# Performance work log

Hardware: AMD Instinct MI355X
Metric: run time of the kernel (lower is better)

Reference implementation:

```python
import jax, jax.numpy as jnp
import numpy as np


def setup_inputs() -> dict:
    key = jax.random.key(0)
    k1, k2 = jax.random.split(key)
    G, T, H, E, C = 8, 4096, 1024, 32, 64
    token_inputs = jax.random.normal(k1, (G, T, H), dtype=jnp.float32)
    W = jax.random.normal(k2, (H, E), dtype=jnp.float32) * 0.02  # default_kernel_init stddev
    b = jnp.zeros((E,), dtype=jnp.float32)
    return {"token_inputs": token_inputs, "W": W, "b": b,
            "num_experts": E, "expert_capacity": C}


def reference(token_inputs, W, b, num_experts, expert_capacity):
    # RouterWeights: dense projection to expert logits, computed in fp32.
    x = token_inputs.astype(jnp.float32)                      # [G, T, H]
    router_logits = jnp.einsum('gth,he->gte', x, W) + b        # [G, T, E]
    router_probs = jax.nn.softmax(router_logits, axis=-1)      # [G, T, E]

    # Experts-choose masked routing: each expert picks its top-C tokens.
    probs_et = jnp.swapaxes(router_probs, 1, 2)                # [G, E, T]
    gate, idx = jax.lax.top_k(probs_et, expert_capacity)       # [G, E, C]

    T = token_inputs.shape[1]
    # one-hot over the token axis -> dispatch mask [G, T, E, C]
    dispatch = jax.nn.one_hot(idx, T, dtype=jnp.float32)       # [G, E, C, T]
    dispatch = jnp.transpose(dispatch, (0, 3, 1, 2))           # [G, T, E, C]
    combine = dispatch * gate[:, None, :, :]                   # [G, T, E, C]

    # Router z-loss on raw logits.
    G_, T_, _ = router_logits.shape
    log_z = jax.nn.logsumexp(router_logits, axis=-1)           # [G, T]
    z_loss = jnp.sum(jnp.square(log_z), dtype=jnp.float32) / (G_ * T_)
    return combine, dispatch, z_loss
```

## Files before the change

kernel.cpp:

```cpp
#include <hip/hip_runtime.h>
#include <math.h>

#define G 8
#define T 4096
#define H 1024
#define E 32
#define C 64
#define NTOK (G*T)
#define COMBINE_SZ ((size_t)G*T*E*C)
#define KC 64
#define TBLK 128

__global__ __launch_bounds__(256) void k_router(
    const float* __restrict__ x, const float* __restrict__ W,
    const float* __restrict__ bias, float* __restrict__ probs_t,
    float* __restrict__ z_out)
{
    __shared__ float xs[TBLK][68];
    __shared__ float ws2[KC][32];
    __shared__ float lt[TBLK][33];

    const int tid  = threadIdx.x;
    const int lane = tid & 63;
    const int wv   = __builtin_amdgcn_readfirstlane(tid >> 6);
    const int blk  = blockIdx.x;

    float acc0[8] = {0,0,0,0,0,0,0,0};
    float acc1[8] = {0,0,0,0,0,0,0,0};

    for (int ch = 0; ch < H / KC; ++ch) {
        const int h0 = ch * KC;

        {
            const float4* __restrict__ src = (const float4*)(W + (size_t)h0 * E);
            float4* __restrict__ dst = (float4*)ws2;
            dst[tid]       = src[tid];
            dst[tid + 256] = src[tid + 256];
        }
        #pragma unroll
        for (int k = 0; k < 8; ++k) {
            const int f   = k * 256 + tid;
            const int tok = f >> 4;
            const int h4  = f & 15;
            const float4 v = *(const float4*)(x + (size_t)(blk * TBLK + tok) * H + h0 + h4 * 4);
            *(float4*)(&xs[tok][h4 * 4]) = v;
        }
        __syncthreads();

        for (int hh = 0; hh < KC; hh += 4) {
            const float4 xa = *(const float4*)(&xs[lane][hh]);
            const float4 xb = *(const float4*)(&xs[64 + lane][hh]);
            #pragma unroll
            for (int j = 0; j < 4; ++j) {
                const float4 w0 = *(const float4*)(&ws2[hh + j][wv * 8]);
                const float4 w1 = *(const float4*)(&ws2[hh + j][wv * 8 + 4]);
                const float a_ = (j == 0) ? xa.x : (j == 1) ? xa.y : (j == 2) ? xa.z : xa.w;
                const float b_ = (j == 0) ? xb.x : (j == 1) ? xb.y : (j == 2) ? xb.z : xb.w;
                acc0[0] = fmaf(a_, w0.x, acc0[0]);  acc1[0] = fmaf(b_, w0.x, acc1[0]);
                acc0[1] = fmaf(a_, w0.y, acc0[1]);  acc1[1] = fmaf(b_, w0.y, acc1[1]);
                acc0[2] = fmaf(a_, w0.z, acc0[2]);  acc1[2] = fmaf(b_, w0.z, acc1[2]);
                acc0[3] = fmaf(a_, w0.w, acc0[3]);  acc1[3] = fmaf(b_, w0.w, acc1[3]);
                acc0[4] = fmaf(a_, w1.x, acc0[4]);  acc1[4] = fmaf(b_, w1.x, acc1[4]);
                acc0[5] = fmaf(a_, w1.y, acc0[5]);  acc1[5] = fmaf(b_, w1.y, acc1[5]);
                acc0[6] = fmaf(a_, w1.z, acc0[6]);  acc1[6] = fmaf(b_, w1.z, acc1[6]);
                acc0[7] = fmaf(a_, w1.w, acc0[7]);  acc1[7] = fmaf(b_, w1.w, acc1[7]);
            }
        }
        __syncthreads();
    }

    #pragma unroll
    for (int e = 0; e < 8; ++e) {
        const float be = bias[wv * 8 + e];
        lt[lane][wv * 8 + e]      = acc0[e] + be;
        lt[64 + lane][wv * 8 + e] = acc1[e] + be;
    }
    __syncthreads();

    if (tid < TBLK) {
        float v[E];
        float m = -1e30f;
        #pragma unroll
        for (int e = 0; e < E; ++e) { v[e] = lt[tid][e]; m = fmaxf(m, v[e]); }
        float s = 0.f;
        #pragma unroll
        for (int e = 0; e < E; ++e) { v[e] = expf(v[e] - m); s += v[e]; }
        const float inv = 1.f / s;
        #pragma unroll
        for (int e = 0; e < E; ++e) lt[tid][e] = v[e] * inv;
        const float lz = m + logf(s);
        float zsq = lz * lz;
        #pragma unroll
        for (int off = 32; off; off >>= 1) zsq += __shfl_down(zsq, off, 64);
        if ((tid & 63) == 0) atomicAdd(z_out, zsq * (1.0f / (float)NTOK));
    }
    __syncthreads();

    const int g  = blk >> 5;
    const int tb = (blk & 31) * TBLK;
    #pragma unroll
    for (int j = 0; j < 8; ++j) {
        const int e = wv * 8 + j;
        float* __restrict__ col = probs_t + ((size_t)(g * E + e)) * T + tb;
        col[lane]      = lt[lane][e];
        col[64 + lane] = lt[64 + lane][e];
    }
}

__global__ __launch_bounds__(256) void k_topk(
    const float* __restrict__ probs_t, float* __restrict__ out)
{
    const int ge   = blockIdx.x;
    const int g    = ge >> 5;
    const int e    = ge & 31;
    const int tid  = threadIdx.x;
    const int lane = tid & 63;
    const int wv   = tid >> 6;
    const float* __restrict__ col = probs_t + (size_t)ge * T;

    __shared__ unsigned long long sk[T];
    __shared__ unsigned long long wmin[4];
    __shared__ unsigned long long thr_s;
    __shared__ int cnt;

    if (tid == 0) cnt = 0;

    unsigned long long keys[16];
    #pragma unroll
    for (int j = 0; j < 16; ++j) {
        const int t = j * 256 + tid;
        unsigned u = __float_as_uint(col[t]);
        u = (u & 0x80000000u) ? ~u : (u | 0x80000000u);
        keys[j] = ((unsigned long long)u << 32) | (unsigned)(4095 - t);
    }

    unsigned long long tm = keys[0];
    #pragma unroll
    for (int j = 1; j < 16; ++j) tm = (keys[j] > tm) ? keys[j] : tm;
    unsigned long long gm = tm;
    {
        unsigned long long o = __shfl_xor(gm, 1, 64); gm = (o > gm) ? o : gm;
        o = __shfl_xor(gm, 2, 64);                    gm = (o > gm) ? o : gm;
    }
    unsigned long long mn = gm;
    #pragma unroll
    for (int off = 4; off < 64; off <<= 1) {
        const unsigned long long o = __shfl_xor(mn, off, 64);
        mn = (o < mn) ? o : mn;
    }
    if (lane == 0) wmin[wv] = mn;
    __syncthreads();
    if (tid == 0) {
        unsigned long long m = wmin[0];
        #pragma unroll
        for (int w = 1; w < 4; ++w) m = (wmin[w] < m) ? wmin[w] : m;
        thr_s = m;
    }
    __syncthreads();
    const unsigned long long thr = thr_s;

    #pragma unroll
    for (int j = 0; j < 16; ++j) {
        const bool pred = (keys[j] >= thr);
        const unsigned long long mask = __ballot(pred);
        int base = 0;
        if (lane == 0) {
            const int nw = (int)__popcll(mask);
            base = nw ? atomicAdd(&cnt, nw) : 0;
        }
        base = __shfl(base, 0, 64);
        if (pred) {
            const int pos = (int)__popcll(mask & ((1ull << lane) - 1ull));
            sk[base + pos] = keys[j];
        }
    }
    __syncthreads();
    const int n = cnt;

    for (int i = tid; i < n; i += 256) {
        const unsigned long long k = sk[i];
        int r = 0;
        for (int j = 0; j < n; ++j) r += (sk[j] > k) ? 1 : 0;
        if (r < C) {
            const int t = 4095 - (int)(k & 0xFFFFFFFFu);
            const unsigned mu   = (unsigned)(k >> 32);
            const unsigned orig = (mu & 0x80000000u) ? (mu & 0x7FFFFFFFu) : ~mu;
            const size_t idx = ((((size_t)g * T + t) * E + e) * C + r);
            out[idx] = __uint_as_float(orig);
            out[idx + COMBINE_SZ] = 1.0f;
        }
    }
}

extern "C" void kernel_launch(void* const* d_in, const int* in_sizes, int n_in,
                              void* d_out, int out_size, void* d_ws, size_t ws_size,
                              hipStream_t stream) {
    const float* x = (const float*)d_in[0];
    const float* W = (const float*)d_in[1];
    const float* b = (const float*)d_in[2];
    float* out     = (float*)d_out;
    float* probs_t = (float*)d_ws;

    hipMemsetAsync(d_out, 0, (size_t)(2 * COMBINE_SZ + 1) * sizeof(float), stream);

    k_router<<<NTOK / TBLK, 256, 0, stream>>>(x, W, b, probs_t, out + 2 * COMBINE_SZ);
    k_topk<<<G * E, 256, 0, stream>>>(probs_t, out);
}
```

Baseline: 685.7 us.

## Fuse zero-fill of combine/dispatch into top-k kernel, drop full memset

Instead of memsetting the full combine and dispatch tensors and then scattering non-zeros, each top-k block records which tokens it selected, and their ranks, in shared memory. It then writes its whole [T, C] slice of both outputs densely with float4 stores, zeros included. This removes the separate memset pass and the scattered writes, so each output byte is written once. Each block's stores are strided, 256 bytes per token row with a stride of E*C floats, which may coalesce less well than a memset.

```diff
diff --git a/kernel.cpp b/kernel.cpp
--- a/kernel.cpp
+++ b/kernel.cpp
@@ -122,8 +122,15 @@
     __shared__ unsigned long long wmin[4];
     __shared__ unsigned long long thr_s;
     __shared__ int cnt;
+    __shared__ unsigned char sel[T];
+    __shared__ float sgate[C];
 
     if (tid == 0) cnt = 0;
+    {
+        unsigned* p = (unsigned*)sel;
+        #pragma unroll
+        for (int j = 0; j < 4; ++j) p[j * 256 + tid] = 0u;
+    }
 
     unsigned long long keys[16];
     #pragma unroll
@@ -185,9 +192,37 @@
             const int t = 4095 - (int)(k & 0xFFFFFFFFu);
             const unsigned mu   = (unsigned)(k >> 32);
             const unsigned orig = (mu & 0x80000000u) ? (mu & 0x7FFFFFFFu) : ~mu;
-            const size_t idx = ((((size_t)g * T + t) * E + e) * C + r);
-            out[idx] = __uint_as_float(orig);
-            out[idx + COMBINE_SZ] = 1.0f;
+            sel[t]   = (unsigned char)(r + 1);
+            sgate[r] = __uint_as_float(orig);
+        }
+    }
+    __syncthreads();
+
+    {
+        const int tq = tid >> 4;
+        const int c4 = tid & 15;
+        size_t off = (size_t)g * ((size_t)T * E * C)
+                   + (size_t)tq * (E * C)
+                   + (size_t)e * C
+                   + (size_t)(c4 * 4);
+        float* __restrict__ oc = out;
+        float* __restrict__ od = out + COMBINE_SZ;
+        for (int pass = 0; pass < T / 16; ++pass) {
+            const int t = pass * 16 + tq;
+            const int s = (int)sel[t];
+            float4 vc = make_float4(0.f, 0.f, 0.f, 0.f);
+            float4 vd = make_float4(0.f, 0.f, 0.f, 0.f);
+            if (s) {
+                const int c = s - 1;
+                if ((c >> 2) == c4) {
+                    const float gv = sgate[c];
+                    ((float*)&vc)[c & 3] = gv;
+                    ((float*)&vd)[c & 3] = 1.0f;
+                }
+            }
+            *(float4*)(oc + off) = vc;
+            *(float4*)(od + off) = vd;
+            off += (size_t)16 * E * C;
         }
     }
 }
@@ -201,7 +236,7 @@
     float* out     = (float*)d_out;
     float* probs_t = (float*)d_ws;
 
-    hipMemsetAsync(d_out, 0, (size_t)(2 * COMBINE_SZ + 1) * sizeof(float), stream);
+    hipMemsetAsync(out + 2 * COMBINE_SZ, 0, sizeof(float), stream);
 
     k_router<<<NTOK / TBLK, 256, 0, stream>>>(x, W, b, probs_t, out + 2 * COMBINE_SZ);
     k_topk<<<G * E, 256, 0, stream>>>(probs_t, out);
```

Measured after the change: 753.8 us. 9.9% more time.

## Replace full-output memset with per-row dense writer using selection lists

Applied to the files above, without the earlier changes.

Rather than memsetting the whole 2×G·T·E·C output and then scattering sparse values, the top-k kernel now records each selected (expert, slot) pair in a per-token list. A new write kernel then streams every output row once with nontemporal float4 stores, filling in the gates and ones. This removes the separate memset pass and the scattered writes, at the cost of an extra kernel, atomics on per-token counters, and workspace space. If the workspace is too small, the old path is kept as a fallback.

```diff
diff --git a/kernel.cpp b/kernel.cpp
--- a/kernel.cpp
+++ b/kernel.cpp
@@ -11,6 +11,12 @@
 #define KC 64
 #define TBLK 128
 
+typedef float f4_t __attribute__((ext_vector_type(4)));
+
+__device__ __forceinline__ void nt_store4(float* p, f4_t v) {
+    __builtin_nontemporal_store(v, (f4_t*)p);
+}
+
 __global__ __launch_bounds__(256) void k_router(
     const float* __restrict__ x, const float* __restrict__ W,
     const float* __restrict__ bias, float* __restrict__ probs_t,
@@ -30,7 +36,6 @@
 
     for (int ch = 0; ch < H / KC; ++ch) {
         const int h0 = ch * KC;
-
         {
             const float4* __restrict__ src = (const float4*)(W + (size_t)h0 * E);
             float4* __restrict__ dst = (float4*)ws2;
@@ -107,7 +112,133 @@
     }
 }
 
-__global__ __launch_bounds__(256) void k_topk(
+__global__ __launch_bounds__(256) void k_select(
+    const float* __restrict__ probs_t, unsigned* __restrict__ cnt,
+    unsigned short* __restrict__ ec)
+{
+    const int ge   = blockIdx.x;
+    const int g    = ge >> 5;
+    const int e    = ge & 31;
+    const int tid  = threadIdx.x;
+    const int lane = tid & 63;
+    const int wv   = tid >> 6;
+    const float* __restrict__ col = probs_t + (size_t)ge * T;
+
+    __shared__ unsigned long long sk[T];
+    __shared__ unsigned long long wmin[4];
+    __shared__ unsigned long long thr_s;
+    __shared__ int scnt;
+
+    if (tid == 0) scnt = 0;
+
+    unsigned long long keys[16];
+    #pragma unroll
+    for (int j = 0; j < 16; ++j) {
+        const int t = j * 256 + tid;
+        unsigned u = __float_as_uint(col[t]);
+        u = (u & 0x80000000u) ? ~u : (u | 0x80000000u);
+        keys[j] = ((unsigned long long)u << 32) | (unsigned)(4095 - t);
+    }
+
+    unsigned long long tm = keys[0];
+    #pragma unroll
+    for (int j = 1; j < 16; ++j) tm = (keys[j] > tm) ? keys[j] : tm;
+    unsigned long long gm = tm;
+    {
+        unsigned long long o = __shfl_xor(gm, 1, 64); gm = (o > gm) ? o : gm;
+        o = __shfl_xor(gm, 2, 64);                    gm = (o > gm) ? o : gm;
+    }
+    unsigned long long mn = gm;
+    #pragma unroll
+    for (int off = 4; off < 64; off <<= 1) {
+        const unsigned long long o = __shfl_xor(mn, off, 64);
+        mn = (o < mn) ? o : mn;
+    }
+    if (lane == 0) wmin[wv] = mn;
+    __syncthreads();
+    if (tid == 0) {
+        unsigned long long m = wmin[0];
+        #pragma unroll
+        for (int w = 1; w < 4; ++w) m = (wmin[w] < m) ? wmin[w] : m;
+        thr_s = m;
+    }
+    __syncthreads();
+    const unsigned long long thr = thr_s;
+
+    #pragma unroll
+    for (int j = 0; j < 16; ++j) {
+        const bool pred = (keys[j] >= thr);
+        const unsigned long long mask = __ballot(pred);
+        int base = 0;
+        if (lane == 0) {
+            const int nw = (int)__popcll(mask);
+            base = nw ? atomicAdd(&scnt, nw) : 0;
+        }
+        base = __shfl(base, 0, 64);
+        if (pred) {
+            const int pos = (int)__popcll(mask & ((1ull << lane) - 1ull));
+            sk[base + pos] = keys[j];
+        }
+    }
+    __syncthreads();
+    const int n = scnt;
+
+    for (int i = tid; i < n; i += 256) {
+        const unsigned long long k = sk[i];
+        int r = 0;
+        for (int j = 0; j < n; ++j) r += (sk[j] > k) ? 1 : 0;
+        if (r < C) {
+            const int t = 4095 - (int)(k & 0xFFFFFFFFu);
+            const int row = g * T + t;
+            const unsigned pos = atomicAdd(&cnt[row], 1u);
+            ec[((size_t)row << 5) + pos] = (unsigned short)((e << 6) | r);
+        }
+    }
+}
+
+__global__ __launch_bounds__(256) void k_write(
+    const float* __restrict__ probs_t, const unsigned* __restrict__ cnt,
+    const unsigned short* __restrict__ ec, float* __restrict__ out)
+{
+    const int lane = threadIdx.x & 63;
+    const int wid  = (blockIdx.x << 2) | (threadIdx.x >> 6);
+    const int nw   = gridDim.x << 2;
+    const f4_t z4  = (f4_t){0.f, 0.f, 0.f, 0.f};
+
+    for (int row = wid; row < G * T; row += nw) {
+        const int g = row >> 12;
+        const int t = row & (T - 1);
+        const int n = (int)cnt[row];
+        float* __restrict__ oc = out + (size_t)row * (E * C);
+        float* __restrict__ od = out + COMBINE_SZ + (size_t)row * (E * C);
+
+        if (n == 0) {
+            #pragma unroll
+            for (int s = 0; s < 8; ++s) {
+                nt_store4(oc + (s * 64 + lane) * 4, z4);
+                nt_store4(od + (s * 64 + lane) * 4, z4);
+            }
+        } else {
+            for (int s = 0; s < 8; ++s) {
+                const int idx = s * 64 + lane;
+                f4_t vc = z4, vd = z4;
+                for (int j = 0; j < n; ++j) {
+                    const unsigned v = (unsigned)ec[((size_t)row << 5) + j];
+                    const int e = (int)(v >> 6), c = (int)(v & 63u);
+                    if ((e * 16 + (c >> 2)) == idx) {
+                        const float gv = probs_t[((size_t)(g * E + e)) * T + t];
+                        vc[c & 3] = gv;
+                        vd[c & 3] = 1.0f;
+                    }
+                }
+                nt_store4(oc + idx * 4, vc);
+                nt_store4(od + idx * 4, vd);
+            }
+        }
+    }
+}
+
+__global__ __launch_bounds__(256) void k_topk_fb(
     const float* __restrict__ probs_t, float* __restrict__ out)
 {
     const int ge   = blockIdx.x;
@@ -121,9 +252,9 @@
     __shared__ unsigned long long sk[T];
     __shared__ unsigned long long wmin[4];
     __shared__ unsigned long long thr_s;
-    __shared__ int cnt;
-
-    if (tid == 0) cnt = 0;
+    __shared__ int scnt;
+
+    if (tid == 0) scnt = 0;
 
     unsigned long long keys[16];
     #pragma unroll
@@ -133,7 +264,6 @@
         u = (u & 0x80000000u) ? ~u : (u | 0x80000000u);
         keys[j] = ((unsigned long long)u << 32) | (unsigned)(4095 - t);
     }
-
     unsigned long long tm = keys[0];
     #pragma unroll
     for (int j = 1; j < 16; ++j) tm = (keys[j] > tm) ? keys[j] : tm;
@@ -166,7 +296,7 @@
         int base = 0;
         if (lane == 0) {
             const int nw = (int)__popcll(mask);
-            base = nw ? atomicAdd(&cnt, nw) : 0;
+            base = nw ? atomicAdd(&scnt, nw) : 0;
         }
         base = __shfl(base, 0, 64);
         if (pred) {
@@ -175,7 +305,7 @@
         }
     }
     __syncthreads();
-    const int n = cnt;
+    const int n = scnt;
 
     for (int i = tid; i < n; i += 256) {
         const unsigned long long k = sk[i];
@@ -201,8 +331,23 @@
     float* out     = (float*)d_out;
     float* probs_t = (float*)d_ws;
 
-    hipMemsetAsync(d_out, 0, (size_t)(2 * COMBINE_SZ + 1) * sizeof(float), stream);
-
-    k_router<<<NTOK / TBLK, 256, 0, stream>>>(x, W, b, probs_t, out + 2 * COMBINE_SZ);
-    k_topk<<<G * E, 256, 0, stream>>>(probs_t, out);
-}
+    const size_t cnt_off = (size_t)4 * 1024 * 1024;
+    const size_t ec_off  = cnt_off + (size_t)G * T * 4;
+    const size_t need    = ec_off + (size_t)G * T * 32 * 2;
+
+    if (ws_size >= need) {
+        unsigned*       cnt = (unsigned*)((char*)d_ws + cnt_off);
+        unsigned short* ec  = (unsigned short*)((char*)d_ws + ec_off);
+
+        hipMemsetAsync(cnt, 0, (size_t)G * T * 4, stream);
+        hipMemsetAsync(out + 2 * COMBINE_SZ, 0, sizeof(float), stream);
+
+        k_router<<<NTOK / TBLK, 256, 0, stream>>>(x, W, b, probs_t, out + 2 * COMBINE_SZ);
+        k_select<<<G * E, 256, 0, stream>>>(probs_t, cnt, ec);
+        k_write<<<2048, 256, 0, stream>>>(probs_t, cnt, ec, out);
+    } else {
+        hipMemsetAsync(d_out, 0, (size_t)(2 * COMBINE_SZ + 1) * sizeof(float), stream);
+        k_router<<<NTOK / TBLK, 256, 0, stream>>>(x, W, b, probs_t, out + 2 * COMBINE_SZ);
+        k_topk_fb<<<G * E, 256, 0, stream>>>(probs_t, out);
+    }
+}
```

After: 710.0 us. 1.04x slower.
